# Kernel tuning notes

Measured on AMD Instinct MI355X. Metric: run time of the kernel, lower is better.

The kernel has to match this reference:

```python
import jax, jax.numpy as jnp
import numpy as np

K_PER_CLASS = 10
WINDOW = 7
MIN_MASS = 0.05
EPS = 1e-8


def _pool_sum(x, w):
    # sum-pool over last two dims, stride 1, zero padding w//2 (count_include_pad avg = sum / w^2)
    nd = x.ndim
    return jax.lax.reduce_window(
        x, 0.0, jax.lax.add,
        (1,) * (nd - 2) + (w, w),
        (1,) * nd,
        [(0, 0)] * (nd - 2) + [(w // 2, w // 2)] * 2,
    )


def _l2norm(x, axis):
    # matches torch F.normalize(p=2): x / max(||x||, 1e-12)
    return x / jnp.maximum(jnp.linalg.norm(x, axis=axis, keepdims=True), 1e-12)


def setup_inputs() -> dict:
    key = jax.random.key(0)
    k1, k2, k3 = jax.random.split(key, 3)
    feature_map = jax.random.normal(k1, (8, 512, 96, 96), dtype=jnp.float32)
    prototypes = jax.random.normal(k2, (80, 512), dtype=jnp.float32)
    pseudo_mask = jax.random.randint(k3, (8, 96, 96), 0, 9, dtype=jnp.int32)
    return {"feature_map": feature_map, "prototypes": prototypes, "pseudo_mask": pseudo_mask}


def reference(feature_map, prototypes, pseudo_mask):
    B, D, H, W = feature_map.shape
    K = K_PER_CLASS
    C = prototypes.shape[0] // K
    area = WINDOW * WINDOW

    Fn = _l2norm(feature_map, 1)                       # [B,D,H,W]
    Pn = _l2norm(prototypes, 1).reshape(C, K, D)       # [C,K,D]
    sim = jnp.einsum('bdhw,ckd->bckhw', Fn, Pn)        # [B,C,K,H,W]

    omega = (pseudo_mask[:, None] == (jnp.arange(C) + 1)[None, :, None, None]).astype(sim.dtype)  # [B,C,H,W]

    num = _pool_sum(sim * omega[:, :, None], WINDOW) / area   # [B,C,K,H,W]
    den = _pool_sum(omega, WINDOW) / area                      # [B,C,H,W]
    region = num / (den[:, :, None] + EPS)

    a = region.reshape(B, C, K, H * W).transpose(0, 1, 3, 2)   # [B,C,HW,K]
    valid = (den > MIN_MASS).reshape(B, C, H * W)
    V = valid.sum(-1)                                          # [B,C] int
    Vf = jnp.maximum(V, 1).astype(a.dtype)
    vm = valid[..., None].astype(a.dtype)

    mean = (a * vm).sum(2) / Vf[..., None]                     # [B,C,K]
    a_c = (a - mean[:, :, None]) * vm                          # zero out invalid rows
    nrm = jnp.sqrt((a_c * a_c).sum(2))                         # [B,C,K]
    a_n = a_c / (nrm[:, :, None] + EPS)

    gram = jnp.einsum('bcvk,bcvl->bckl', a_n, a_n) / Vf[..., None, None]  # [B,C,K,K]
    off = gram * (1.0 - jnp.eye(K, dtype=gram.dtype))
    loss_c = (off * off).sum((-1, -2)) / (K * (K - 1))         # [B,C]

    active = (omega.sum((-1, -2)) >= 1.0) & (V >= 2)           # mirrors skip conditions
    af = active.astype(loss_c.dtype)
    per_image = (loss_c * af).sum(-1) / jnp.maximum(af.sum(-1), 1.0)
    return per_image.sum() / B
```

## Files before the change

### kernel.cpp

```cpp
#include <hip/hip_runtime.h>
#include <cstdint>
#include <cstddef>

namespace {
constexpr int Bn = 8, Dn = 512, Hn = 96, Wn = 96, HWn = Hn * Wn;
constexpr int Cn = 8, Kn = 10, CKn = Cn * Kn;
constexpr int NPIX = Bn * HWn;
constexpr int NCHUNK = 4, DCH = Dn / NCHUNK;
constexpr int NMOM = 66;
constexpr float EPSF = 1e-8f;
constexpr float MINM = 0.05f;

constexpr size_t oPnT  = 0;
constexpr size_t oS    = oPnT + (size_t)Dn * CKn;
constexpr size_t oNumH = oS + (size_t)Bn * Kn * HWn;
constexpr size_t oPart = oNumH;
constexpr size_t oDenH = oNumH + (size_t)Bn * Cn * Kn * HWn;
constexpr size_t oMom  = oDenH + (size_t)Bn * Cn * HWn;
constexpr size_t oCnt  = oMom + 64 * NMOM;
constexpr size_t oEnd  = oCnt + 64;
}

__device__ __forceinline__ float wred64(float v) {
#pragma unroll
    for (int o = 32; o > 0; o >>= 1) v += __shfl_down(v, o, 64);
    return v;
}

__global__ __launch_bounds__(64) void k_protonorm(const float* __restrict__ P,
                                                  float* __restrict__ PnT) {
    int ck = blockIdx.x, lane = threadIdx.x;
    float v[8]; float ss = 0.f;
#pragma unroll
    for (int j = 0; j < 8; ++j) { v[j] = P[ck * Dn + lane + 64 * j]; ss += v[j] * v[j]; }
    ss = wred64(ss);
    ss = __shfl(ss, 0, 64);
    float inv = 1.0f / fmaxf(sqrtf(ss), 1e-12f);
#pragma unroll
    for (int j = 0; j < 8; ++j)
        PnT[(size_t)(lane + 64 * j) * CKn + ck] = v[j] * inv;
}

__global__ __launch_bounds__(256) void k_sim(const float* __restrict__ F,
                                             const float* __restrict__ PnT,
                                             const int* __restrict__ mask,
                                             float* __restrict__ part) {
    __shared__ float pch[64 * 96];
    const int tid = threadIdx.x;
    const int pix = blockIdx.x * 256 + tid;
    const int chunk = blockIdx.y;
    const int b = pix / HWn, hw = pix % HWn;

    const int m = mask[pix];
    const int cc = m > 0 ? m - 1 : 0;

    float acc[Kn]; float ss = 0.f;
#pragma unroll
    for (int k = 0; k < Kn; ++k) acc[k] = 0.f;

    for (int p = 0; p < DCH / 64; ++p) {
        const int dbase = chunk * DCH + p * 64;
        __syncthreads();
        for (int i = tid; i < 64 * CKn; i += 256) {
            int dd = i / CKn, ck = i % CKn;
            int c = ck / Kn, kk = ck % Kn;
            pch[dd * 96 + c * 12 + kk] = PnT[(size_t)(dbase + dd) * CKn + ck];
        }
        __syncthreads();
#pragma unroll 4
        for (int dd = 0; dd < 64; ++dd) {
            float f = F[(size_t)(b * Dn + dbase + dd) * HWn + hw];
            ss += f * f;
            const float4* p4 = (const float4*)&pch[dd * 96 + cc * 12];
            float4 pa = p4[0], pb = p4[1];
            float2 pc = *(const float2*)&pch[dd * 96 + cc * 12 + 8];
            acc[0] += f * pa.x; acc[1] += f * pa.y; acc[2] += f * pa.z; acc[3] += f * pa.w;
            acc[4] += f * pb.x; acc[5] += f * pb.y; acc[6] += f * pb.z; acc[7] += f * pb.w;
            acc[8] += f * pc.x; acc[9] += f * pc.y;
        }
    }
#pragma unroll
    for (int k = 0; k < Kn; ++k)
        part[(size_t)(chunk * 11 + k) * NPIX + pix] = acc[k];
    part[(size_t)(chunk * 11 + 10) * NPIX + pix] = ss;
}

__global__ __launch_bounds__(256) void k_simred(const float* __restrict__ part,
                                                const int* __restrict__ mask,
                                                float* __restrict__ S,
                                                int* __restrict__ cnt) {
    __shared__ int hist[Cn];
    const int tid = threadIdx.x;
    const int pix = blockIdx.x * 256 + tid;
    if (tid < Cn) hist[tid] = 0;
    __syncthreads();

    float acc[Kn]; float ss = 0.f;
#pragma unroll
    for (int k = 0; k < Kn; ++k) acc[k] = 0.f;
#pragma unroll
    for (int ch = 0; ch < NCHUNK; ++ch) {
#pragma unroll
        for (int k = 0; k < Kn; ++k)
            acc[k] += part[(size_t)(ch * 11 + k) * NPIX + pix];
        ss += part[(size_t)(ch * 11 + 10) * NPIX + pix];
    }
    float inv = 1.0f / fmaxf(sqrtf(ss), 1e-12f);
    const int b = pix / HWn, hw = pix % HWn;
#pragma unroll
    for (int k = 0; k < Kn; ++k)
        S[(size_t)(b * Kn + k) * HWn + hw] = acc[k] * inv;

    const int m = mask[pix];
    if (m > 0) atomicAdd(&hist[m - 1], 1);
    __syncthreads();
    if (tid < Cn) atomicAdd(&cnt[(pix / HWn) * Cn + tid], hist[tid]);
}

__global__ __launch_bounds__(256) void k_hpool(const int* __restrict__ mask,
                                               const float* __restrict__ S,
                                               float* __restrict__ numH,
                                               float* __restrict__ denH) {
    const int t = blockIdx.x * 256 + threadIdx.x;
    const int wg = t % 24;
    int r = t / 24;
    const int h = r % Hn; r /= Hn;
    const int k2 = r % 5;
    const int bc = r / 5;
    const int c = bc & 7, b = bc >> 3;
    const int k0 = 2 * k2;
    const int w0 = wg * 4;
    const int rowb = b * HWn + h * Wn;
    const float* S0 = &S[(size_t)(b * Kn + k0) * HWn + h * Wn];
    const float* S1 = &S[(size_t)(b * Kn + k0 + 1) * HWn + h * Wn];

    float a0[4] = {0.f, 0.f, 0.f, 0.f};
    float a1[4] = {0.f, 0.f, 0.f, 0.f};
    float dn[4] = {0.f, 0.f, 0.f, 0.f};

#pragma unroll
    for (int dc = -3; dc <= 6; ++dc) {
        int ww = w0 + dc;
        if (ww < 0 || ww >= Wn) continue;
        float hv = (mask[rowb + ww] == c + 1) ? 1.0f : 0.0f;
        float s0 = S0[ww] * hv;
        float s1 = S1[ww] * hv;
        const int olo = dc - 3 > 0 ? dc - 3 : 0;
        const int ohi = dc + 3 < 3 ? dc + 3 : 3;
#pragma unroll
        for (int o = 0; o < 4; ++o) {
            if (o < olo || o > ohi) continue;
            a0[o] += s0; a1[o] += s1; dn[o] += hv;
        }
    }
    float4* n0 = (float4*)&numH[(size_t)(bc * Kn + k0) * HWn + h * Wn + w0];
    float4* n1 = (float4*)&numH[(size_t)(bc * Kn + k0 + 1) * HWn + h * Wn + w0];
    *n0 = make_float4(a0[0], a0[1], a0[2], a0[3]);
    *n1 = make_float4(a1[0], a1[1], a1[2], a1[3]);
    if (k2 == 0)
        *(float4*)&denH[(size_t)bc * HWn + h * Wn + w0] =
            make_float4(dn[0], dn[1], dn[2], dn[3]);
}

__global__ __launch_bounds__(256) void k_vpool(const float* __restrict__ numH,
                                               const float* __restrict__ denH,
                                               float* __restrict__ mom) {
    const int t = blockIdx.x * 256 + threadIdx.x;
    const int w = t % Wn;
    int r = t / Wn;
    const int hg = r % 24;
    const int bc = r / 24;
    const int h0 = hg * 4;

    float nacc[4][Kn];
    float dacc[4] = {0.f, 0.f, 0.f, 0.f};
#pragma unroll
    for (int o = 0; o < 4; ++o)
#pragma unroll
        for (int k = 0; k < Kn; ++k) nacc[o][k] = 0.f;

#pragma unroll
    for (int dr = -3; dr <= 6; ++dr) {
        int hh = h0 + dr;
        if (hh < 0 || hh >= Hn) continue;
        const int olo = dr - 3 > 0 ? dr - 3 : 0;
        const int ohi = dr + 3 < 3 ? dr + 3 : 3;
        float dv = denH[(size_t)bc * HWn + hh * Wn + w];
#pragma unroll
        for (int o = 0; o < 4; ++o) {
            if (o < olo || o > ohi) continue;
            dacc[o] += dv;
        }
#pragma unroll
        for (int k = 0; k < Kn; ++k) {
            float nv = numH[(size_t)(bc * Kn + k) * HWn + hh * Wn + w];
#pragma unroll
            for (int o = 0; o < 4; ++o) {
                if (o < olo || o > ohi) continue;
                nacc[o][k] += nv;
            }
        }
    }

    float m[NMOM];
#pragma unroll
    for (int i = 0; i < NMOM; ++i) m[i] = 0.f;
#pragma unroll
    for (int o = 0; o < 4; ++o) {
        float dA = dacc[o] * (1.0f / 49.0f);
        float inv = 1.0f / (dA + EPSF);
        float vm = (dA > MINM) ? 1.0f : 0.0f;
        float rr[Kn];
#pragma unroll
        for (int k = 0; k < Kn; ++k)
            rr[k] = nacc[o][k] * (1.0f / 49.0f) * inv * vm;
        m[0] += vm;
#pragma unroll
        for (int k = 0; k < Kn; ++k) m[1 + k] += rr[k];
        int p = 11;
#pragma unroll
        for (int k = 0; k < Kn; ++k)
#pragma unroll
            for (int l = 0; l <= k; ++l, ++p) m[p] += rr[k] * rr[l];
    }

    __shared__ float red[4][NMOM];
    const int lane = threadIdx.x & 63, wv = threadIdx.x >> 6;
#pragma unroll
    for (int i = 0; i < NMOM; ++i) {
        float x = wred64(m[i]);
        if (lane == 0) red[wv][i] = x;
    }
    __syncthreads();
    for (int i = threadIdx.x; i < NMOM; i += 256)
        atomicAdd(&mom[bc * NMOM + i],
                  red[0][i] + red[1][i] + red[2][i] + red[3][i]);
}

__global__ __launch_bounds__(64) void k_final(const float* __restrict__ mom,
                                              const int* __restrict__ cnt,
                                              float* __restrict__ out) {
    const int bc = threadIdx.x;
    float mo[NMOM];
#pragma unroll
    for (int i = 0; i < NMOM; ++i) mo[i] = mom[bc * NMOM + i];
    const float V = mo[0];
    const float Vf = fmaxf(V, 1.0f);
    float Sk[Kn];
#pragma unroll
    for (int k = 0; k < Kn; ++k) Sk[k] = mo[1 + k];

    float M[55];
    {
        int p = 0;
#pragma unroll
        for (int k = 0; k < Kn; ++k)
#pragma unroll
            for (int l = 0; l <= k; ++l, ++p)
                M[p] = mo[11 + p] - Sk[k] * Sk[l] / Vf;
    }
    float nrm[Kn];
#pragma unroll
    for (int k = 0; k < Kn; ++k)
        nrm[k] = sqrtf(fmaxf(M[k * (k + 1) / 2 + k], 0.0f));
    float loss = 0.f;
    {
        int p = 0;
#pragma unroll
        for (int k = 0; k < Kn; ++k) {
#pragma unroll
            for (int l = 0; l <= k; ++l, ++p) {
                if (l == k) continue;
                float g = M[p] / ((nrm[k] + EPSF) * (nrm[l] + EPSF)) / Vf;
                loss += 2.0f * g * g;
            }
        }
    }
    loss *= 1.0f / (float)(Kn * (Kn - 1));
    bool act = (cnt[bc] >= 1) && (V >= 2.0f);
    float sl = act ? loss : 0.f;
    float sa = act ? 1.f : 0.f;
#pragma unroll
    for (int o = 4; o > 0; o >>= 1) {
        sl += __shfl_down(sl, o, 8);
        sa += __shfl_down(sa, o, 8);
    }
    __shared__ float pimg[Bn];
    if ((bc & 7) == 0) pimg[bc >> 3] = sl / fmaxf(sa, 1.0f);
    __syncthreads();
    if (bc == 0) {
        float tot = 0.f;
#pragma unroll
        for (int b = 0; b < Bn; ++b) tot += pimg[b];
        out[0] = tot / (float)Bn;
    }
}

extern "C" void kernel_launch(void* const* d_in, const int* in_sizes, int n_in,
                              void* d_out, int out_size, void* d_ws, size_t ws_size,
                              hipStream_t stream) {
    const float* F  = (const float*)d_in[0];
    const float* P  = (const float*)d_in[1];
    const int* mask = (const int*)d_in[2];
    float* ws = (float*)d_ws;
    float* out = (float*)d_out;

    hipMemsetAsync(ws + oMom, 0, (oEnd - oMom) * sizeof(float), stream);

    k_protonorm<<<CKn, 64, 0, stream>>>(P, ws + oPnT);
    k_sim<<<dim3(NPIX / 256, NCHUNK), 256, 0, stream>>>(F, ws + oPnT, mask, ws + oPart);
    k_simred<<<NPIX / 256, 256, 0, stream>>>(ws + oPart, mask, ws + oS, (int*)(ws + oCnt));
    k_hpool<<<Bn * Cn * 5 * Hn * 24 / 256, 256, 0, stream>>>(mask, ws + oS,
                                                             ws + oNumH, ws + oDenH);
    k_vpool<<<Bn * Cn * 24 * Wn / 256, 256, 0, stream>>>(ws + oNumH, ws + oDenH, ws + oMom);
    k_final<<<1, 64, 0, stream>>>(ws + oMom, (const int*)(ws + oCnt), out);
}
```

Baseline: 286.0 us.

## Fuse sim reduction into k_sim and merge horizontal/vertical pooling via shared memory

The similarity kernel now splits the D dimension across four wavefronts inside one block and reduces the partial sums in shared memory, which removes the separate partial-sum buffer and the k_simred launch. The two pooling passes are merged into one kernel that computes horizontal sums for a strip of rows plus halo into LDS, then does the vertical sums and moment accumulation from LDS. This removes the large numH/denH global round trip. In exchange, halo rows are recomputed per strip and LDS use rises, which may limit occupancy.

```diff
diff --git a/kernel.cpp b/kernel.cpp
--- a/kernel.cpp
+++ b/kernel.cpp
@@ -6,19 +6,16 @@
 constexpr int Bn = 8, Dn = 512, Hn = 96, Wn = 96, HWn = Hn * Wn;
 constexpr int Cn = 8, Kn = 10, CKn = Cn * Kn;
 constexpr int NPIX = Bn * HWn;
-constexpr int NCHUNK = 4, DCH = Dn / NCHUNK;
 constexpr int NMOM = 66;
+constexpr int RSTRIP = 8;
 constexpr float EPSF = 1e-8f;
 constexpr float MINM = 0.05f;
 
-constexpr size_t oPnT  = 0;
-constexpr size_t oS    = oPnT + (size_t)Dn * CKn;
-constexpr size_t oNumH = oS + (size_t)Bn * Kn * HWn;
-constexpr size_t oPart = oNumH;
-constexpr size_t oDenH = oNumH + (size_t)Bn * Cn * Kn * HWn;
-constexpr size_t oMom  = oDenH + (size_t)Bn * Cn * HWn;
-constexpr size_t oCnt  = oMom + 64 * NMOM;
-constexpr size_t oEnd  = oCnt + 64;
+constexpr size_t oPnT = 0;
+constexpr size_t oS   = oPnT + (size_t)Dn * CKn;
+constexpr size_t oMom = oS + (size_t)Bn * Kn * HWn;
+constexpr size_t oCnt = oMom + 64 * NMOM;
+constexpr size_t oEnd = oCnt + 64;
 }
 
 __device__ __forceinline__ float wred64(float v) {
@@ -44,12 +41,16 @@
 __global__ __launch_bounds__(256) void k_sim(const float* __restrict__ F,
                                              const float* __restrict__ PnT,
                                              const int* __restrict__ mask,
-                                             float* __restrict__ part) {
+                                             float* __restrict__ S,
+                                             int* __restrict__ cnt) {
     __shared__ float pch[64 * 96];
+    __shared__ int hist[Cn];
     const int tid = threadIdx.x;
-    const int pix = blockIdx.x * 256 + tid;
-    const int chunk = blockIdx.y;
+    const int pixLocal = tid & 63;
+    const int g = tid >> 6;
+    const int pix = blockIdx.x * 64 + pixLocal;
     const int b = pix / HWn, hw = pix % HWn;
+    if (tid < Cn) hist[tid] = 0;
 
     const int m = mask[pix];
     const int cc = m > 0 ? m - 1 : 0;
@@ -58,181 +59,147 @@
 #pragma unroll
     for (int k = 0; k < Kn; ++k) acc[k] = 0.f;
 
-    for (int p = 0; p < DCH / 64; ++p) {
-        const int dbase = chunk * DCH + p * 64;
+    for (int p = 0; p < 8; ++p) {
         __syncthreads();
         for (int i = tid; i < 64 * CKn; i += 256) {
-            int dd = i / CKn, ck = i % CKn;
+            int sd = i / CKn, ck = i % CKn;
+            int sg = sd >> 4, dd = sd & 15;
+            int gd = sg * 128 + p * 16 + dd;
             int c = ck / Kn, kk = ck % Kn;
-            pch[dd * 96 + c * 12 + kk] = PnT[(size_t)(dbase + dd) * CKn + ck];
+            pch[sd * 96 + c * 12 + kk] = PnT[(size_t)gd * CKn + ck];
         }
         __syncthreads();
-#pragma unroll 4
-        for (int dd = 0; dd < 64; ++dd) {
-            float f = F[(size_t)(b * Dn + dbase + dd) * HWn + hw];
+        const float* Fp = &F[(size_t)(b * Dn + g * 128 + p * 16) * HWn + hw];
+#pragma unroll
+        for (int dd = 0; dd < 16; ++dd) {
+            float f = Fp[(size_t)dd * HWn];
             ss += f * f;
-            const float4* p4 = (const float4*)&pch[dd * 96 + cc * 12];
+            const float4* p4 = (const float4*)&pch[(g * 16 + dd) * 96 + cc * 12];
             float4 pa = p4[0], pb = p4[1];
-            float2 pc = *(const float2*)&pch[dd * 96 + cc * 12 + 8];
+            float2 pc = *(const float2*)&pch[(g * 16 + dd) * 96 + cc * 12 + 8];
             acc[0] += f * pa.x; acc[1] += f * pa.y; acc[2] += f * pa.z; acc[3] += f * pa.w;
             acc[4] += f * pb.x; acc[5] += f * pb.y; acc[6] += f * pb.z; acc[7] += f * pb.w;
             acc[8] += f * pc.x; acc[9] += f * pc.y;
         }
     }
-#pragma unroll
-    for (int k = 0; k < Kn; ++k)
-        part[(size_t)(chunk * 11 + k) * NPIX + pix] = acc[k];
-    part[(size_t)(chunk * 11 + 10) * NPIX + pix] = ss;
-}
-
-__global__ __launch_bounds__(256) void k_simred(const float* __restrict__ part,
-                                                const int* __restrict__ mask,
-                                                float* __restrict__ S,
-                                                int* __restrict__ cnt) {
-    __shared__ int hist[Cn];
+    __syncthreads();
+    float* red = pch;
+#pragma unroll
+    for (int k = 0; k < Kn; ++k) red[g * 768 + pixLocal * 12 + k] = acc[k];
+    red[g * 768 + pixLocal * 12 + 10] = ss;
+    __syncthreads();
+    if (tid < 64) {
+        float tot[11];
+#pragma unroll
+        for (int j = 0; j < 11; ++j)
+            tot[j] = red[tid * 12 + j] + red[768 + tid * 12 + j] +
+                     red[1536 + tid * 12 + j] + red[2304 + tid * 12 + j];
+        float inv = 1.0f / fmaxf(sqrtf(tot[10]), 1e-12f);
+#pragma unroll
+        for (int k = 0; k < Kn; ++k)
+            S[(size_t)(b * Kn + k) * HWn + hw] = tot[k] * inv;
+        if (m > 0) atomicAdd(&hist[m - 1], 1);
+    }
+    __syncthreads();
+    if (tid < Cn) atomicAdd(&cnt[((blockIdx.x * 64) / HWn) * Cn + tid], hist[tid]);
+}
+
+__global__ __launch_bounds__(256) void k_pool(const int* __restrict__ mask,
+                                              const float* __restrict__ S,
+                                              float* __restrict__ mom) {
+    __shared__ float sNum[Kn][14 * 96];
+    __shared__ float sDen[14 * 96];
+    __shared__ float red[4][NMOM];
+    const int bc = blockIdx.x / 12, strip = blockIdx.x % 12;
+    const int c = bc & 7, b = bc >> 3;
+    const int h0 = strip * RSTRIP;
     const int tid = threadIdx.x;
-    const int pix = blockIdx.x * 256 + tid;
-    if (tid < Cn) hist[tid] = 0;
-    __syncthreads();
-
-    float acc[Kn]; float ss = 0.f;
-#pragma unroll
-    for (int k = 0; k < Kn; ++k) acc[k] = 0.f;
-#pragma unroll
-    for (int ch = 0; ch < NCHUNK; ++ch) {
-#pragma unroll
-        for (int k = 0; k < Kn; ++k)
-            acc[k] += part[(size_t)(ch * 11 + k) * NPIX + pix];
-        ss += part[(size_t)(ch * 11 + 10) * NPIX + pix];
-    }
-    float inv = 1.0f / fmaxf(sqrtf(ss), 1e-12f);
-    const int b = pix / HWn, hw = pix % HWn;
-#pragma unroll
-    for (int k = 0; k < Kn; ++k)
-        S[(size_t)(b * Kn + k) * HWn + hw] = acc[k] * inv;
-
-    const int m = mask[pix];
-    if (m > 0) atomicAdd(&hist[m - 1], 1);
-    __syncthreads();
-    if (tid < Cn) atomicAdd(&cnt[(pix / HWn) * Cn + tid], hist[tid]);
-}
-
-__global__ __launch_bounds__(256) void k_hpool(const int* __restrict__ mask,
-                                               const float* __restrict__ S,
-                                               float* __restrict__ numH,
-                                               float* __restrict__ denH) {
-    const int t = blockIdx.x * 256 + threadIdx.x;
-    const int wg = t % 24;
-    int r = t / 24;
-    const int h = r % Hn; r /= Hn;
-    const int k2 = r % 5;
-    const int bc = r / 5;
-    const int c = bc & 7, b = bc >> 3;
-    const int k0 = 2 * k2;
-    const int w0 = wg * 4;
-    const int rowb = b * HWn + h * Wn;
-    const float* S0 = &S[(size_t)(b * Kn + k0) * HWn + h * Wn];
-    const float* S1 = &S[(size_t)(b * Kn + k0 + 1) * HWn + h * Wn];
-
-    float a0[4] = {0.f, 0.f, 0.f, 0.f};
-    float a1[4] = {0.f, 0.f, 0.f, 0.f};
-    float dn[4] = {0.f, 0.f, 0.f, 0.f};
-
-#pragma unroll
-    for (int dc = -3; dc <= 6; ++dc) {
-        int ww = w0 + dc;
-        if (ww < 0 || ww >= Wn) continue;
-        float hv = (mask[rowb + ww] == c + 1) ? 1.0f : 0.0f;
-        float s0 = S0[ww] * hv;
-        float s1 = S1[ww] * hv;
-        const int olo = dc - 3 > 0 ? dc - 3 : 0;
-        const int ohi = dc + 3 < 3 ? dc + 3 : 3;
+
+    for (int item = tid; item < 14 * 24; item += 256) {
+        const int r = item / 24, wg = item % 24;
+        const int hh = h0 - 3 + r;
+        const int w0 = wg * 4;
+        float a[Kn][4];
+        float dn[4] = {0.f, 0.f, 0.f, 0.f};
+#pragma unroll
+        for (int k = 0; k < Kn; ++k)
+#pragma unroll
+            for (int o = 0; o < 4; ++o) a[k][o] = 0.f;
+
+        if (hh >= 0 && hh < Hn) {
+            const int rowb = b * HWn + hh * Wn;
+            const float* Srow = &S[(size_t)b * Kn * HWn + hh * Wn];
+#pragma unroll
+            for (int dc = -3; dc <= 6; ++dc) {
+                int ww = w0 + dc;
+                if (ww < 0 || ww >= Wn) continue;
+                const int olo = dc - 3 > 0 ? dc - 3 : 0;
+                const int ohi = dc + 3 < 3 ? dc + 3 : 3;
+                if (mask[rowb + ww] == c + 1) {
+#pragma unroll
+                    for (int o = 0; o < 4; ++o)
+                        if (o >= olo && o <= ohi) dn[o] += 1.0f;
+#pragma unroll
+                    for (int k = 0; k < Kn; ++k) {
+                        float s = Srow[(size_t)k * HWn + ww];
+#pragma unroll
+                        for (int o = 0; o < 4; ++o)
+                            if (o >= olo && o <= ohi) a[k][o] += s;
+                    }
+                }
+            }
+        }
 #pragma unroll
         for (int o = 0; o < 4; ++o) {
-            if (o < olo || o > ohi) continue;
-            a0[o] += s0; a1[o] += s1; dn[o] += hv;
-        }
-    }
-    float4* n0 = (float4*)&numH[(size_t)(bc * Kn + k0) * HWn + h * Wn + w0];
-    float4* n1 = (float4*)&numH[(size_t)(bc * Kn + k0 + 1) * HWn + h * Wn + w0];
-    *n0 = make_float4(a0[0], a0[1], a0[2], a0[3]);
-    *n1 = make_float4(a1[0], a1[1], a1[2], a1[3]);
-    if (k2 == 0)
-        *(float4*)&denH[(size_t)bc * HWn + h * Wn + w0] =
-            make_float4(dn[0], dn[1], dn[2], dn[3]);
-}
-
-__global__ __launch_bounds__(256) void k_vpool(const float* __restrict__ numH,
-                                               const float* __restrict__ denH,
-                                               float* __restrict__ mom) {
-    const int t = blockIdx.x * 256 + threadIdx.x;
-    const int w = t % Wn;
-    int r = t / Wn;
-    const int hg = r % 24;
-    const int bc = r / 24;
-    const int h0 = hg * 4;
-
-    float nacc[4][Kn];
-    float dacc[4] = {0.f, 0.f, 0.f, 0.f};
-#pragma unroll
-    for (int o = 0; o < 4; ++o)
-#pragma unroll
-        for (int k = 0; k < Kn; ++k) nacc[o][k] = 0.f;
-
-#pragma unroll
-    for (int dr = -3; dr <= 6; ++dr) {
-        int hh = h0 + dr;
-        if (hh < 0 || hh >= Hn) continue;
-        const int olo = dr - 3 > 0 ? dr - 3 : 0;
-        const int ohi = dr + 3 < 3 ? dr + 3 : 3;
-        float dv = denH[(size_t)bc * HWn + hh * Wn + w];
-#pragma unroll
-        for (int o = 0; o < 4; ++o) {
-            if (o < olo || o > ohi) continue;
-            dacc[o] += dv;
-        }
-#pragma unroll
-        for (int k = 0; k < Kn; ++k) {
-            float nv = numH[(size_t)(bc * Kn + k) * HWn + hh * Wn + w];
-#pragma unroll
-            for (int o = 0; o < 4; ++o) {
-                if (o < olo || o > ohi) continue;
-                nacc[o][k] += nv;
-            }
-        }
-    }
-
-    float m[NMOM];
-#pragma unroll
-    for (int i = 0; i < NMOM; ++i) m[i] = 0.f;
-#pragma unroll
-    for (int o = 0; o < 4; ++o) {
-        float dA = dacc[o] * (1.0f / 49.0f);
+            sDen[r * 96 + w0 + o] = dn[o];
+#pragma unroll
+            for (int k = 0; k < Kn; ++k) sNum[k][r * 96 + w0 + o] = a[k][o];
+        }
+    }
+    __syncthreads();
+
+    float mm[NMOM];
+#pragma unroll
+    for (int i = 0; i < NMOM; ++i) mm[i] = 0.f;
+
+    for (int out = tid; out < RSTRIP * 96; out += 256) {
+        const int oh = out / 96, w = out % 96;
+        float den = 0.f;
+        float n[Kn];
+#pragma unroll
+        for (int k = 0; k < Kn; ++k) n[k] = 0.f;
+#pragma unroll
+        for (int dr = 0; dr < 7; ++dr) {
+            const int r = oh + dr;
+            den += sDen[r * 96 + w];
+#pragma unroll
+            for (int k = 0; k < Kn; ++k) n[k] += sNum[k][r * 96 + w];
+        }
+        float dA = den * (1.0f / 49.0f);
         float inv = 1.0f / (dA + EPSF);
         float vm = (dA > MINM) ? 1.0f : 0.0f;
         float rr[Kn];
 #pragma unroll
         for (int k = 0; k < Kn; ++k)
-            rr[k] = nacc[o][k] * (1.0f / 49.0f) * inv * vm;
-        m[0] += vm;
-#pragma unroll
-        for (int k = 0; k < Kn; ++k) m[1 + k] += rr[k];
+            rr[k] = n[k] * (1.0f / 49.0f) * inv * vm;
+        mm[0] += vm;
+#pragma unroll
+        for (int k = 0; k < Kn; ++k) mm[1 + k] += rr[k];
         int p = 11;
 #pragma unroll
         for (int k = 0; k < Kn; ++k)
 #pragma unroll
-            for (int l = 0; l <= k; ++l, ++p) m[p] += rr[k] * rr[l];
-    }
-
-    __shared__ float red[4][NMOM];
-    const int lane = threadIdx.x & 63, wv = threadIdx.x >> 6;
+            for (int l = 0; l <= k; ++l, ++p) mm[p] += rr[k] * rr[l];
+    }
+
+    const int lane = tid & 63, wv = tid >> 6;
 #pragma unroll
     for (int i = 0; i < NMOM; ++i) {
-        float x = wred64(m[i]);
+        float x = wred64(mm[i]);
         if (lane == 0) red[wv][i] = x;
     }
     __syncthreads();
-    for (int i = threadIdx.x; i < NMOM; i += 256)
+    for (int i = tid; i < NMOM; i += 256)
         atomicAdd(&mom[bc * NMOM + i],
                   red[0][i] + red[1][i] + red[2][i] + red[3][i]);
 }
@@ -308,10 +275,8 @@
     hipMemsetAsync(ws + oMom, 0, (oEnd - oMom) * sizeof(float), stream);
 
     k_protonorm<<<CKn, 64, 0, stream>>>(P, ws + oPnT);
-    k_sim<<<dim3(NPIX / 256, NCHUNK), 256, 0, stream>>>(F, ws + oPnT, mask, ws + oPart);
-    k_simred<<<NPIX / 256, 256, 0, stream>>>(ws + oPart, mask, ws + oS, (int*)(ws + oCnt));
-    k_hpool<<<Bn * Cn * 5 * Hn * 24 / 256, 256, 0, stream>>>(mask, ws + oS,
-                                                             ws + oNumH, ws + oDenH);
-    k_vpool<<<Bn * Cn * 24 * Wn / 256, 256, 0, stream>>>(ws + oNumH, ws + oDenH, ws + oMom);
+    k_sim<<<NPIX / 64, 256, 0, stream>>>(F, ws + oPnT, mask, ws + oS,
+                                         (int*)(ws + oCnt));
+    k_pool<<<64 * 12, 256, 0, stream>>>(mask, ws + oS, ws + oMom);
     k_final<<<1, 64, 0, stream>>>(ws + oMom, (const int*)(ws + oCnt), out);
 }
```

Result: slower. 319.8 us (+11.8%).
